# Kernel optimization log

Measured on AMD Instinct MI355X. Metric: run time of the kernel, lower is better.

The kernel has to match this reference:

```python
import jax, jax.numpy as jnp
import numpy as np

D = 1024
H = 16
F = 4096
EPS = 1e-6


def _layernorm(x, alpha, bias):
    # Faithful to torch: unbiased std (ddof=1), divide by (std + eps)
    mean = jnp.mean(x, axis=-1, keepdims=True)
    std = jnp.std(x, axis=-1, keepdims=True, ddof=1)
    return alpha * (x - mean) / (std + EPS) + bias


def setup_inputs() -> dict:
    key = jax.random.key(0)
    ks = jax.random.split(key, 12)
    B, S = 2, 2048
    s = 1.0 / np.sqrt(D)
    inp = {
        "x": jax.random.normal(ks[0], (B, S, D), jnp.float32),
        "mask": jnp.ones((B, 1, 1, S), jnp.int32),
        "wq": jax.random.normal(ks[1], (D, D), jnp.float32) * s,
        "bq": jnp.zeros((D,), jnp.float32),
        "wk": jax.random.normal(ks[2], (D, D), jnp.float32) * s,
        "bk": jnp.zeros((D,), jnp.float32),
        "wv": jax.random.normal(ks[3], (D, D), jnp.float32) * s,
        "bv": jnp.zeros((D,), jnp.float32),
        "wo": jax.random.normal(ks[4], (D, D), jnp.float32) * s,
        "bo": jnp.zeros((D,), jnp.float32),
        "ln1_a": jnp.ones((D,), jnp.float32),
        "ln1_b": jnp.zeros((D,), jnp.float32),
        "ln2_a": jnp.ones((D,), jnp.float32),
        "ln2_b": jnp.zeros((D,), jnp.float32),
        "w1": jax.random.normal(ks[5], (D, F), jnp.float32) * s,
        "b1": jnp.zeros((F,), jnp.float32),
        "w2": jax.random.normal(ks[6], (F, D), jnp.float32) * (1.0 / np.sqrt(F)),
        "b2": jnp.zeros((D,), jnp.float32),
    }
    return inp


def reference(x, mask, wq, bq, wk, bk, wv, bv, wo, bo,
              ln1_a, ln1_b, ln2_a, ln2_b, w1, b1, w2, b2):
    B, S, _ = x.shape
    dk = D // H
    # --- residual 1: pre-LN self-attention ---
    h = _layernorm(x, ln1_a, ln1_b)
    q = (h @ wq + bq).reshape(B, S, H, dk).transpose(0, 2, 1, 3)
    k = (h @ wk + bk).reshape(B, S, H, dk).transpose(0, 2, 1, 3)
    v = (h @ wv + bv).reshape(B, S, H, dk).transpose(0, 2, 1, 3)
    scores = jnp.einsum('bhqd,bhkd->bhqk', q, k) / jnp.sqrt(jnp.float32(dk))
    scores = jnp.where(mask == 0, jnp.float32(-1e9), scores)
    attn = jax.nn.softmax(scores, axis=-1)
    ctx = jnp.einsum('bhqk,bhkd->bhqd', attn, v)
    ctx = ctx.transpose(0, 2, 1, 3).reshape(B, S, D)
    x = x + (ctx @ wo + bo)
    # --- residual 2: pre-LN feed-forward ---
    h = _layernorm(x, ln2_a, ln2_b)
    ff = jax.nn.relu(h @ w1 + b1) @ w2 + b2
    return x + ff
```

## Files before the change

### kernel.cpp

```cpp
#include <hip/hip_runtime.h>
#include <hip/hip_bf16.h>

typedef __attribute__((ext_vector_type(8))) short bf16x8;
typedef __attribute__((ext_vector_type(4))) float f32x4;
typedef unsigned int uint32;

#define DMODEL 1024
#define SEQ    2048
#define NB     2
#define NH     16
#define HD     64
#define FDIM   4096
#define NTOK   (NB*SEQ)

__device__ __forceinline__ void async16(const void* g, void* s) {
    __builtin_amdgcn_global_load_lds((const __attribute__((address_space(1))) unsigned int*)g,
                                     (__attribute__((address_space(3))) unsigned int*)s,
                                     16, 0, 0);
}

__global__ __launch_bounds__(256) void transpose_cvt_k(const float* __restrict__ src,
                                                       __hip_bfloat16* __restrict__ dst,
                                                       int R, int C) {
    __shared__ __hip_bfloat16 tile[32][33];
    int tx = threadIdx.x, ty = threadIdx.y;
    int bx = blockIdx.x * 32, by = blockIdx.y * 32;
    for (int i = 0; i < 32; i += 8)
        tile[ty + i][tx] = __float2bfloat16(src[(size_t)(by + ty + i) * C + bx + tx]);
    __syncthreads();
    for (int i = 0; i < 32; i += 8)
        dst[(size_t)(bx + ty + i) * R + by + tx] = tile[tx][ty + i];
}

__global__ __launch_bounds__(256) void ln_kernel(const float* __restrict__ x,
                                                 const float* __restrict__ alpha,
                                                 const float* __restrict__ beta,
                                                 __hip_bfloat16* __restrict__ out) {
    const int row = blockIdx.x, tid = threadIdx.x;
    const size_t base = (size_t)row * DMODEL;
    float v[4];
    for (int e = 0; e < 4; ++e) v[e] = x[base + tid * 4 + e];
    float s1 = v[0] + v[1] + v[2] + v[3];
    float s2 = v[0]*v[0] + v[1]*v[1] + v[2]*v[2] + v[3]*v[3];
    for (int off = 32; off > 0; off >>= 1) {
        s1 += __shfl_down(s1, off);
        s2 += __shfl_down(s2, off);
    }
    __shared__ float red[8];
    int w = tid >> 6, lane = tid & 63;
    if (lane == 0) { red[w * 2] = s1; red[w * 2 + 1] = s2; }
    __syncthreads();
    if (tid == 0) {
        float a = 0.f, b = 0.f;
        for (int i = 0; i < 4; ++i) { a += red[2 * i]; b += red[2 * i + 1]; }
        red[0] = a; red[1] = b;
    }
    __syncthreads();
    s1 = red[0]; s2 = red[1];
    float mean = s1 * (1.0f / DMODEL);
    float var  = fmaxf((s2 - (float)DMODEL * mean * mean) * (1.0f / (DMODEL - 1)), 0.f);
    float inv  = 1.0f / (sqrtf(var) + 1e-6f);
    for (int e = 0; e < 4; ++e) {
        int c = tid * 4 + e;
        float y = alpha[c] * (v[e] - mean) * inv + beta[c];
        out[base + c] = __float2bfloat16(y);
    }
}

template <int EPI>
__global__ __launch_bounds__(256) void gemm_bt(const __hip_bfloat16* __restrict__ A,
                                               const __hip_bfloat16* __restrict__ Bt,
                                               const float* __restrict__ bias,
                                               const float* __restrict__ res,
                                               void* __restrict__ Cout,
                                               int M, int N, int K) {
    __shared__ alignas(16) __hip_bfloat16 As[2][128 * 32];
    __shared__ alignas(16) __hip_bfloat16 Bs[2][128 * 32];
    const int tid = threadIdx.x, l = tid & 63;
    const int w = tid >> 6;
    const int wm = w >> 1, wn = w & 1, quad = l >> 4, lc = l & 15;
    const int row0 = blockIdx.y * 128, col0 = blockIdx.x * 128;
    const int srow = 32 * w + (l >> 2), scol = (l & 3) * 8;

    f32x4 acc[4][4];
    for (int i = 0; i < 4; ++i)
        for (int j = 0; j < 4; ++j) acc[i][j] = (f32x4){0.f, 0.f, 0.f, 0.f};

    for (int c = 0; c < 2; ++c) {
        async16(A  + (size_t)(row0 + srow + 16 * c) * K + scol, (char*)&As[0][0] + w * 2048 + c * 1024);
        async16(Bt + (size_t)(col0 + srow + 16 * c) * K + scol, (char*)&Bs[0][0] + w * 2048 + c * 1024);
    }
    const int NKT = K / 32;
    for (int kt = 0; kt < NKT; ++kt) {
        const int cur = kt & 1;
        __syncthreads();
        if (kt + 1 < NKT) {
            const int k1 = (kt + 1) * 32;
            for (int c = 0; c < 2; ++c) {
                async16(A  + (size_t)(row0 + srow + 16 * c) * K + k1 + scol, (char*)&As[cur ^ 1][0] + w * 2048 + c * 1024);
                async16(Bt + (size_t)(col0 + srow + 16 * c) * K + k1 + scol, (char*)&Bs[cur ^ 1][0] + w * 2048 + c * 1024);
            }
        }
        bf16x8 af[4], bfr[4];
        for (int i = 0; i < 4; ++i) af[i]  = *(const bf16x8*)&As[cur][(64 * wm + 16 * i + lc) * 32 + quad * 8];
        for (int j = 0; j < 4; ++j) bfr[j] = *(const bf16x8*)&Bs[cur][(64 * wn + 16 * j + lc) * 32 + quad * 8];
        for (int i = 0; i < 4; ++i)
            for (int j = 0; j < 4; ++j)
                acc[i][j] = __builtin_amdgcn_mfma_f32_16x16x32_bf16(af[i], bfr[j], acc[i][j], 0, 0, 0);
    }

    __hip_bfloat16* Cb = (__hip_bfloat16*)Cout;
    float* Cf = (float*)Cout;
    for (int j = 0; j < 4; ++j) {
        int col = col0 + 64 * wn + 16 * j + lc;
        float bv = bias[col];
        for (int i = 0; i < 4; ++i) {
            int rbase = row0 + 64 * wm + 16 * i + quad * 4;
            for (int r = 0; r < 4; ++r) {
                size_t idx = (size_t)(rbase + r) * N + col;
                float vacc = acc[i][j][r] + bv;
                if (EPI == 0)      Cb[idx] = __float2bfloat16(vacc);
                else if (EPI == 1) Cb[idx] = __float2bfloat16(fmaxf(vacc, 0.f));
                else               Cf[idx] = vacc + res[idx];
            }
        }
    }
}

__global__ __launch_bounds__(256) void gemm_qkv(const __hip_bfloat16* __restrict__ A,
                                                const __hip_bfloat16* __restrict__ Bt,
                                                const float* __restrict__ bq,
                                                const float* __restrict__ bk,
                                                const float* __restrict__ bv,
                                                __hip_bfloat16* __restrict__ qout,
                                                __hip_bfloat16* __restrict__ kout,
                                                __hip_bfloat16* __restrict__ vTout) {
    const int K = DMODEL;
    __shared__ alignas(16) __hip_bfloat16 As[2][128 * 32];
    __shared__ alignas(16) __hip_bfloat16 Bs[2][128 * 32];
    const int tid = threadIdx.x, l = tid & 63;
    const int w = tid >> 6;
    const int wm = w >> 1, wn = w & 1, quad = l >> 4, lc = l & 15;
    const int row0 = blockIdx.y * 128, col0 = blockIdx.x * 128;
    const int srow = 32 * w + (l >> 2), scol = (l & 3) * 8;

    f32x4 acc[4][4];
    for (int i = 0; i < 4; ++i)
        for (int j = 0; j < 4; ++j) acc[i][j] = (f32x4){0.f, 0.f, 0.f, 0.f};

    for (int c = 0; c < 2; ++c) {
        async16(A  + (size_t)(row0 + srow + 16 * c) * K + scol, (char*)&As[0][0] + w * 2048 + c * 1024);
        async16(Bt + (size_t)(col0 + srow + 16 * c) * K + scol, (char*)&Bs[0][0] + w * 2048 + c * 1024);
    }
    const int NKT = K / 32;
    for (int kt = 0; kt < NKT; ++kt) {
        const int cur = kt & 1;
        __syncthreads();
        if (kt + 1 < NKT) {
            const int k1 = (kt + 1) * 32;
            for (int c = 0; c < 2; ++c) {
                async16(A  + (size_t)(row0 + srow + 16 * c) * K + k1 + scol, (char*)&As[cur ^ 1][0] + w * 2048 + c * 1024);
                async16(Bt + (size_t)(col0 + srow + 16 * c) * K + k1 + scol, (char*)&Bs[cur ^ 1][0] + w * 2048 + c * 1024);
            }
        }
        bf16x8 af[4], bfr[4];
        for (int i = 0; i < 4; ++i) af[i]  = *(const bf16x8*)&As[cur][(64 * wm + 16 * i + lc) * 32 + quad * 8];
        for (int j = 0; j < 4; ++j) bfr[j] = *(const bf16x8*)&Bs[cur][(64 * wn + 16 * j + lc) * 32 + quad * 8];
        for (int i = 0; i < 4; ++i)
            for (int j = 0; j < 4; ++j)
                acc[i][j] = __builtin_amdgcn_mfma_f32_16x16x32_bf16(af[i], bfr[j], acc[i][j], 0, 0, 0);
    }

    const int seg = col0 >> 10;
    const float* bias = (seg == 0) ? bq : (seg == 1) ? bk : bv;
    for (int j = 0; j < 4; ++j) {
        int col  = col0 + 64 * wn + 16 * j + lc;
        int colm = col & (DMODEL - 1);
        float bvx = bias[colm];
        for (int i = 0; i < 4; ++i) {
            int rbase = row0 + 64 * wm + 16 * i + quad * 4;
            for (int r = 0; r < 4; ++r) {
                int trow = rbase + r;
                float vacc = acc[i][j][r] + bvx;
                if (seg == 2) {
                    int bb = trow >> 11, s = trow & (SEQ - 1);
                    int hh = colm >> 6, d = colm & (HD - 1);
                    vTout[((size_t)(bb * NH + hh) * HD + d) * SEQ + s] = __float2bfloat16(vacc);
                } else {
                    __hip_bfloat16* dst = (seg == 0) ? qout : kout;
                    dst[(size_t)trow * DMODEL + colm] = __float2bfloat16(vacc);
                }
            }
        }
    }
}

__global__ __launch_bounds__(256) void attn_kernel(const __hip_bfloat16* __restrict__ q,
                                                   const __hip_bfloat16* __restrict__ k,
                                                   const __hip_bfloat16* __restrict__ vT,
                                                   const int* __restrict__ mask,
                                                   __hip_bfloat16* __restrict__ ctx) {
    const int qt = blockIdx.x, bh = blockIdx.y;
    const int b = bh >> 4;
    const int q0 = qt * 128;
    const int tid = threadIdx.x, w = tid >> 6, l = tid & 63, quad = l >> 4, lc = l & 15;

    __shared__ alignas(16) __hip_bfloat16 Kh[2][2][64 * 32];
    __shared__ alignas(16) __hip_bfloat16 Vh[2][2][64 * 32];

    const size_t base   = (size_t)b * SEQ * DMODEL + (size_t)(bh & 15) * HD;
    const size_t vtbase = (size_t)bh * HD * SEQ;

    bf16x8 qf[2][2];
    for (int s = 0; s < 2; ++s) {
        const __hip_bfloat16* qrow = &q[base + (size_t)(q0 + s * 64 + w * 16 + lc) * DMODEL];
        qf[s][0] = *(const bf16x8*)&qrow[quad * 8];
        qf[s][1] = *(const bf16x8*)&qrow[32 + quad * 8];
    }

    f32x4 o[2][4];
    for (int s = 0; s < 2; ++s)
        for (int dj = 0; dj < 4; ++dj) o[s][dj] = (f32x4){0.f, 0.f, 0.f, 0.f};
    float rsp2[2] = {0.f, 0.f};

    const int lr  = l >> 2, cb = l & 3;
    const int cbsw = ((cb ^ ((lr >> 1) & 3))) * 8;
    const int rsw  = (lc >> 1) & 3;
    const int b1v = (l >> 5) & 1, b0v = (l >> 4) & 1;

    for (int c = 0; c < 2; ++c) {
        const int W = w * 2 + c;
        const int rr = (W & 3) * 16 + lr, cc8 = (W >> 2) * 32 + cbsw;
        async16(&k [base   + (size_t)rr * DMODEL + cc8], (char*)&Kh[0][0][0] + W * 1024);
        async16(&vT[vtbase + (size_t)rr * SEQ + cc8],    (char*)&Vh[0][0][0] + W * 1024);
    }

    const int NT = SEQ / 64;
    for (int kt = 0; kt < NT; ++kt) {
        const int k0 = kt * 64;
        const int cur = kt & 1;

        __syncthreads();
        if (kt + 1 < NT) {
            const int k1 = k0 + 64;
            for (int c = 0; c < 2; ++c) {
                const int W = w * 2 + c;
                const int rr = (W & 3) * 16 + lr, cc8 = (W >> 2) * 32 + cbsw;
                async16(&k [base   + (size_t)(k1 + rr) * DMODEL + cc8], (char*)&Kh[cur ^ 1][0][0] + W * 1024);
                async16(&vT[vtbase + (size_t)rr * SEQ + k1 + cc8],      (char*)&Vh[cur ^ 1][0][0] + W * 1024);
            }
        }
        int4 mc[4];
        for (int jn = 0; jn < 4; ++jn)
            mc[jn] = *(const int4*)&mask[b * SEQ + k0 + jn * 16 + quad * 4];

        bf16x8 kf0[4], kf1[4];
        for (int jn = 0; jn < 4; ++jn) {
            kf0[jn] = *(const bf16x8*)&Kh[cur][0][(jn * 16 + lc) * 32 + (quad ^ rsw) * 8];
            kf1[jn] = *(const bf16x8*)&Kh[cur][1][(jn * 16 + lc) * 32 + (quad ^ rsw) * 8];
        }
        bf16x8 vf0[4], vf1[4];
        for (int dj = 0; dj < 4; ++dj) {
            vf0[dj] = *(const bf16x8*)&Vh[cur][0][(dj * 16 + lc) * 32 + (quad ^ rsw) * 8];
            vf1[dj] = *(const bf16x8*)&Vh[cur][1][(dj * 16 + lc) * 32 + (quad ^ rsw) * 8];
        }

        for (int s = 0; s < 2; ++s) {
            f32x4 sa[4];
            __builtin_amdgcn_s_setprio(1);
            for (int jn = 0; jn < 4; ++jn) {
                f32x4 z = (f32x4){0.f, 0.f, 0.f, 0.f};
                z = __builtin_amdgcn_mfma_f32_16x16x32_bf16(kf0[jn], qf[s][0], z, 0, 0, 0);
                z = __builtin_amdgcn_mfma_f32_16x16x32_bf16(kf1[jn], qf[s][1], z, 0, 0, 0);
                sa[jn] = z;
            }
            __builtin_amdgcn_s_setprio(0);

            uint32 wd[4][2];
            float accs = 0.f;
            for (int jn = 0; jn < 4; ++jn) {
                float p0 = mc[jn].x ? __expf(sa[jn][0] * 0.125f) : 0.f;
                float p1 = mc[jn].y ? __expf(sa[jn][1] * 0.125f) : 0.f;
                float p2 = mc[jn].z ? __expf(sa[jn][2] * 0.125f) : 0.f;
                float p3 = mc[jn].w ? __expf(sa[jn][3] * 0.125f) : 0.f;
                accs += (p0 + p1) + (p2 + p3);
                __hip_bfloat16 h0 = __float2bfloat16(p0), h1 = __float2bfloat16(p1);
                __hip_bfloat16 h2 = __float2bfloat16(p2), h3 = __float2bfloat16(p3);
                wd[jn][0] = (uint32)*(unsigned short*)&h0 | ((uint32)*(unsigned short*)&h1 << 16);
                wd[jn][1] = (uint32)*(unsigned short*)&h2 | ((uint32)*(unsigned short*)&h3 << 16);
            }
            rsp2[s] += accs;

            uint32 send1[4], kept[4];
            send1[0] = b1v ? wd[0][0] : wd[1][0];  kept[0] = b1v ? wd[1][0] : wd[0][0];
            send1[1] = b1v ? wd[0][1] : wd[1][1];  kept[1] = b1v ? wd[1][1] : wd[0][1];
            send1[2] = b1v ? wd[2][0] : wd[3][0];  kept[2] = b1v ? wd[3][0] : wd[2][0];
            send1[3] = b1v ? wd[2][1] : wd[3][1];  kept[3] = b1v ? wd[3][1] : wd[2][1];
            uint32 recv1[4];
            for (int t = 0; t < 4; ++t) recv1[t] = (uint32)__shfl_xor((int)send1[t], 32);
            uint32 send2[4], stay[4];
            for (int t = 0; t < 4; ++t) {
                send2[t] = (b1v == b0v) ? recv1[t] : kept[t];
                stay[t]  = (b1v == b0v) ? kept[t]  : recv1[t];
            }
            uint32 recv2[4];
            for (int t = 0; t < 4; ++t) recv2[t] = (uint32)__shfl_xor((int)send2[t], 16);
            uint32 G0[4], G1[4];
            for (int t = 0; t < 4; ++t) {
                G0[t] = b0v ? recv2[t] : stay[t];
                G1[t] = b0v ? stay[t]  : recv2[t];
            }
            union { uint32 u[4]; bf16x8 v8; } pf0, pf1;
            pf0.u[0] = G0[0]; pf0.u[1] = G0[1]; pf0.u[2] = G1[0]; pf0.u[3] = G1[1];
            pf1.u[0] = G0[2]; pf1.u[1] = G0[3]; pf1.u[2] = G1[2]; pf1.u[3] = G1[3];

            __builtin_amdgcn_s_setprio(1);
            for (int dj = 0; dj < 4; ++dj) {
                o[s][dj] = __builtin_amdgcn_mfma_f32_16x16x32_bf16(pf0.v8, vf0[dj], o[s][dj], 0, 0, 0);
                o[s][dj] = __builtin_amdgcn_mfma_f32_16x16x32_bf16(pf1.v8, vf1[dj], o[s][dj], 0, 0, 0);
            }
            __builtin_amdgcn_s_setprio(0);
        }
    }

    for (int s = 0; s < 2; ++s) {
        float rs = rsp2[s];
        rs += __shfl_xor(rs, 16);
        rs += __shfl_xor(rs, 32);
        for (int r = 0; r < 4; ++r) {
            float rq = __shfl(rs, (l & 48) | (quad * 4 + r));
            float linv = 1.0f / rq;
            int row = q0 + s * 64 + w * 16 + quad * 4 + r;
            for (int dj = 0; dj < 4; ++dj)
                ctx[base + (size_t)row * DMODEL + dj * 16 + lc] = __float2bfloat16(o[s][dj][r] * linv);
        }
    }
}

extern "C" void kernel_launch(void* const* d_in, const int* in_sizes, int n_in,
                              void* d_out, int out_size, void* d_ws, size_t ws_size,
                              hipStream_t stream) {
    const float* x    = (const float*)d_in[0];
    const int*   mask = (const int*)d_in[1];
    const float* wq = (const float*)d_in[2];
    const float* bq = (const float*)d_in[3];
    const float* wk = (const float*)d_in[4];
    const float* bk = (const float*)d_in[5];
    const float* wv = (const float*)d_in[6];
    const float* bv = (const float*)d_in[7];
    const float* wo = (const float*)d_in[8];
    const float* bo = (const float*)d_in[9];
    const float* ln1_a = (const float*)d_in[10];
    const float* ln1_b = (const float*)d_in[11];
    const float* ln2_a = (const float*)d_in[12];
    const float* ln2_b = (const float*)d_in[13];
    const float* w1 = (const float*)d_in[14];
    const float* b1 = (const float*)d_in[15];
    const float* w2 = (const float*)d_in[16];
    const float* b2 = (const float*)d_in[17];
    float* out = (float*)d_out;

    char* ws = (char*)d_ws;
    const size_t SZ_WT  = (size_t)DMODEL * DMODEL * 2;
    const size_t SZ_ACT = (size_t)NTOK * DMODEL * 2;
    const size_t SZ_WF  = (size_t)FDIM * DMODEL * 2;
    size_t off = 0;
    __hip_bfloat16* wqkvT = (__hip_bfloat16*)(ws + off); off += 3 * SZ_WT;
    __hip_bfloat16* woT   = (__hip_bfloat16*)(ws + off); off += SZ_WT;
    __hip_bfloat16* w1T   = (__hip_bfloat16*)(ws + off); off += SZ_WF;
    __hip_bfloat16* w2T   = (__hip_bfloat16*)(ws + off); off += SZ_WF;
    __hip_bfloat16* h1    = (__hip_bfloat16*)(ws + off); off += SZ_ACT;
    __hip_bfloat16* qb    = (__hip_bfloat16*)(ws + off); off += SZ_ACT;
    __hip_bfloat16* kb    = (__hip_bfloat16*)(ws + off); off += SZ_ACT;
    __hip_bfloat16* vTb   = (__hip_bfloat16*)(ws + off); off += SZ_ACT;
    __hip_bfloat16* ctx   = (__hip_bfloat16*)(ws + off); off += SZ_ACT;
    float*          x1    = (float*)(ws + off);          off += (size_t)NTOK * DMODEL * 4;
    __hip_bfloat16* h2    = (__hip_bfloat16*)(ws + off); off += SZ_ACT;
    __hip_bfloat16* ff1   = h1;

    dim3 tb(32, 8);
    transpose_cvt_k<<<dim3(32, 32), tb, 0, stream>>>(wq, wqkvT,                   DMODEL, DMODEL);
    transpose_cvt_k<<<dim3(32, 32), tb, 0, stream>>>(wk, wqkvT + 1024 * DMODEL,   DMODEL, DMODEL);
    transpose_cvt_k<<<dim3(32, 32), tb, 0, stream>>>(wv, wqkvT + 2048 * DMODEL,   DMODEL, DMODEL);
    transpose_cvt_k<<<dim3(32, 32), tb, 0, stream>>>(wo, woT, DMODEL, DMODEL);
    transpose_cvt_k<<<dim3(128, 32), tb, 0, stream>>>(w1, w1T, DMODEL, FDIM);
    transpose_cvt_k<<<dim3(32, 128), tb, 0, stream>>>(w2, w2T, FDIM, DMODEL);

    ln_kernel<<<NTOK, 256, 0, stream>>>(x, ln1_a, ln1_b, h1);

    gemm_qkv<<<dim3(3 * DMODEL / 128, NTOK / 128), 256, 0, stream>>>(h1, wqkvT, bq, bk, bv, qb, kb, vTb);

    attn_kernel<<<dim3(SEQ / 128, NB * NH), 256, 0, stream>>>(qb, kb, vTb, mask, ctx);

    gemm_bt<2><<<dim3(DMODEL / 128, NTOK / 128), 256, 0, stream>>>(ctx, woT, bo, x, x1, NTOK, DMODEL, DMODEL);

    ln_kernel<<<NTOK, 256, 0, stream>>>(x1, ln2_a, ln2_b, h2);

    gemm_bt<1><<<dim3(FDIM / 128, NTOK / 128), 256, 0, stream>>>(h2, w1T, b1, nullptr, ff1, NTOK, FDIM, DMODEL);
    gemm_bt<2><<<dim3(DMODEL / 128, NTOK / 128), 256, 0, stream>>>(ff1, w2T, b2, x1, out, NTOK, DMODEL, FDIM);
}
```

Before: 428.1 us.

## Swizzle GEMM LDS layout and split-K the N=1024 GEMMs within a block

Applies an XOR swizzle to the LDS tile layout in the GEMM kernels so the MFMA fragment reads avoid bank conflicts. Adds a 512-thread intra-block split-K GEMM in which two 4-wave groups each process half of K and combine their partial sums through shared memory. It is used for the output projection and the FFN down projection, whose grids have only 256 blocks, to raise the number of active waves. The cost is 64KB of LDS per block, which lowers block residency, plus an extra reduction phase.

```diff
diff --git a/kernel.cpp b/kernel.cpp
--- a/kernel.cpp
+++ b/kernel.cpp
@@ -80,7 +80,10 @@
     const int w = tid >> 6;
     const int wm = w >> 1, wn = w & 1, quad = l >> 4, lc = l & 15;
     const int row0 = blockIdx.y * 128, col0 = blockIdx.x * 128;
-    const int srow = 32 * w + (l >> 2), scol = (l & 3) * 8;
+    const int lr = l >> 2, cb = l & 3;
+    const int srow = 32 * w + lr;
+    const int scol = (cb ^ ((lr >> 1) & 3)) * 8;
+    const int rsw  = (lc >> 1) & 3;
 
     f32x4 acc[4][4];
     for (int i = 0; i < 4; ++i)
@@ -102,8 +105,8 @@
             }
         }
         bf16x8 af[4], bfr[4];
-        for (int i = 0; i < 4; ++i) af[i]  = *(const bf16x8*)&As[cur][(64 * wm + 16 * i + lc) * 32 + quad * 8];
-        for (int j = 0; j < 4; ++j) bfr[j] = *(const bf16x8*)&Bs[cur][(64 * wn + 16 * j + lc) * 32 + quad * 8];
+        for (int i = 0; i < 4; ++i) af[i]  = *(const bf16x8*)&As[cur][(64 * wm + 16 * i + lc) * 32 + (quad ^ rsw) * 8];
+        for (int j = 0; j < 4; ++j) bfr[j] = *(const bf16x8*)&Bs[cur][(64 * wn + 16 * j + lc) * 32 + (quad ^ rsw) * 8];
         for (int i = 0; i < 4; ++i)
             for (int j = 0; j < 4; ++j)
                 acc[i][j] = __builtin_amdgcn_mfma_f32_16x16x32_bf16(af[i], bfr[j], acc[i][j], 0, 0, 0);
@@ -122,6 +125,95 @@
                 if (EPI == 0)      Cb[idx] = __float2bfloat16(vacc);
                 else if (EPI == 1) Cb[idx] = __float2bfloat16(fmaxf(vacc, 0.f));
                 else               Cf[idx] = vacc + res[idx];
+            }
+        }
+    }
+}
+
+template <int EPI>
+__global__ __launch_bounds__(512) void gemm_bt_sk(const __hip_bfloat16* __restrict__ A,
+                                                  const __hip_bfloat16* __restrict__ Bt,
+                                                  const float* __restrict__ bias,
+                                                  const float* __restrict__ res,
+                                                  void* __restrict__ Cout,
+                                                  int M, int N, int K) {
+    __shared__ alignas(16) char smem[65536];
+    const int tid = threadIdx.x, l = tid & 63;
+    const int w = tid >> 6;
+    const int g = w >> 2;
+    const int wl = w & 3;
+    const int wm = wl >> 1, wn = wl & 1, quad = l >> 4, lc = l & 15;
+    const int row0 = blockIdx.y * 128, col0 = blockIdx.x * 128;
+    const int lr = l >> 2, cb = l & 3;
+    const int srow = 32 * wl + lr;
+    const int scol = (cb ^ ((lr >> 1) & 3)) * 8;
+    const int rsw  = (lc >> 1) & 3;
+    const int Kh = K >> 1;
+    const int kbase = g * Kh;
+
+    char* AsBase = smem + (size_t)g * 16384;
+    char* BsBase = smem + 32768 + (size_t)g * 16384;
+
+    f32x4 acc[4][4];
+    for (int i = 0; i < 4; ++i)
+        for (int j = 0; j < 4; ++j) acc[i][j] = (f32x4){0.f, 0.f, 0.f, 0.f};
+
+    for (int c = 0; c < 2; ++c) {
+        async16(A  + (size_t)(row0 + srow + 16 * c) * K + kbase + scol, AsBase + wl * 2048 + c * 1024);
+        async16(Bt + (size_t)(col0 + srow + 16 * c) * K + kbase + scol, BsBase + wl * 2048 + c * 1024);
+    }
+    const int NKT = Kh / 32;
+    for (int kt = 0; kt < NKT; ++kt) {
+        const int cur = kt & 1;
+        __syncthreads();
+        if (kt + 1 < NKT) {
+            const int k1 = kbase + (kt + 1) * 32;
+            for (int c = 0; c < 2; ++c) {
+                async16(A  + (size_t)(row0 + srow + 16 * c) * K + k1 + scol, AsBase + (cur ^ 1) * 8192 + wl * 2048 + c * 1024);
+                async16(Bt + (size_t)(col0 + srow + 16 * c) * K + k1 + scol, BsBase + (cur ^ 1) * 8192 + wl * 2048 + c * 1024);
+            }
+        }
+        const __hip_bfloat16* Asc = (const __hip_bfloat16*)(AsBase + cur * 8192);
+        const __hip_bfloat16* Bsc = (const __hip_bfloat16*)(BsBase + cur * 8192);
+        bf16x8 af[4], bfr[4];
+        for (int i = 0; i < 4; ++i) af[i]  = *(const bf16x8*)&Asc[(64 * wm + 16 * i + lc) * 32 + (quad ^ rsw) * 8];
+        for (int j = 0; j < 4; ++j) bfr[j] = *(const bf16x8*)&Bsc[(64 * wn + 16 * j + lc) * 32 + (quad ^ rsw) * 8];
+        for (int i = 0; i < 4; ++i)
+            for (int j = 0; j < 4; ++j)
+                acc[i][j] = __builtin_amdgcn_mfma_f32_16x16x32_bf16(af[i], bfr[j], acc[i][j], 0, 0, 0);
+    }
+
+    __syncthreads();
+    float* comb = (float*)smem;
+    if (g == 1) {
+        for (int j = 0; j < 4; ++j) {
+            int col = 64 * wn + 16 * j + lc;
+            int ccol = col ^ ((quad & 1) << 4);
+            for (int i = 0; i < 4; ++i) {
+                int rb = 64 * wm + 16 * i + quad * 4;
+                for (int r = 0; r < 4; ++r)
+                    comb[(rb + r) * 128 + ccol] = acc[i][j][r];
+            }
+        }
+    }
+    __syncthreads();
+    if (g == 0) {
+        __hip_bfloat16* Cb = (__hip_bfloat16*)Cout;
+        float* Cf = (float*)Cout;
+        for (int j = 0; j < 4; ++j) {
+            int coll = 64 * wn + 16 * j + lc;
+            int ccol = coll ^ ((quad & 1) << 4);
+            int col  = col0 + coll;
+            float bv = bias[col];
+            for (int i = 0; i < 4; ++i) {
+                int rbl = 64 * wm + 16 * i + quad * 4;
+                for (int r = 0; r < 4; ++r) {
+                    size_t idx = (size_t)(row0 + rbl + r) * N + col;
+                    float vacc = acc[i][j][r] + comb[(rbl + r) * 128 + ccol] + bv;
+                    if (EPI == 0)      Cb[idx] = __float2bfloat16(vacc);
+                    else if (EPI == 1) Cb[idx] = __float2bfloat16(fmaxf(vacc, 0.f));
+                    else               Cf[idx] = vacc + res[idx];
+                }
             }
         }
     }
@@ -142,7 +234,10 @@
     const int w = tid >> 6;
     const int wm = w >> 1, wn = w & 1, quad = l >> 4, lc = l & 15;
     const int row0 = blockIdx.y * 128, col0 = blockIdx.x * 128;
-    const int srow = 32 * w + (l >> 2), scol = (l & 3) * 8;
+    const int lr = l >> 2, cb = l & 3;
+    const int srow = 32 * w + lr;
+    const int scol = (cb ^ ((lr >> 1) & 3)) * 8;
+    const int rsw  = (lc >> 1) & 3;
 
     f32x4 acc[4][4];
     for (int i = 0; i < 4; ++i)
@@ -164,8 +259,8 @@
             }
         }
         bf16x8 af[4], bfr[4];
-        for (int i = 0; i < 4; ++i) af[i]  = *(const bf16x8*)&As[cur][(64 * wm + 16 * i + lc) * 32 + quad * 8];
-        for (int j = 0; j < 4; ++j) bfr[j] = *(const bf16x8*)&Bs[cur][(64 * wn + 16 * j + lc) * 32 + quad * 8];
+        for (int i = 0; i < 4; ++i) af[i]  = *(const bf16x8*)&As[cur][(64 * wm + 16 * i + lc) * 32 + (quad ^ rsw) * 8];
+        for (int j = 0; j < 4; ++j) bfr[j] = *(const bf16x8*)&Bs[cur][(64 * wn + 16 * j + lc) * 32 + (quad ^ rsw) * 8];
         for (int i = 0; i < 4; ++i)
             for (int j = 0; j < 4; ++j)
                 acc[i][j] = __builtin_amdgcn_mfma_f32_16x16x32_bf16(af[i], bfr[j], acc[i][j], 0, 0, 0);
@@ -392,10 +487,10 @@
 
     attn_kernel<<<dim3(SEQ / 128, NB * NH), 256, 0, stream>>>(qb, kb, vTb, mask, ctx);
 
-    gemm_bt<2><<<dim3(DMODEL / 128, NTOK / 128), 256, 0, stream>>>(ctx, woT, bo, x, x1, NTOK, DMODEL, DMODEL);
+    gemm_bt_sk<2><<<dim3(DMODEL / 128, NTOK / 128), 512, 0, stream>>>(ctx, woT, bo, x, x1, NTOK, DMODEL, DMODEL);
 
     ln_kernel<<<NTOK, 256, 0, stream>>>(x1, ln2_a, ln2_b, h2);
 
     gemm_bt<1><<<dim3(FDIM / 128, NTOK / 128), 256, 0, stream>>>(h2, w1T, b1, nullptr, ff1, NTOK, FDIM, DMODEL);
-    gemm_bt<2><<<dim3(DMODEL / 128, NTOK / 128), 256, 0, stream>>>(ff1, w2T, b2, x1, out, NTOK, DMODEL, FDIM);
-}
+    gemm_bt_sk<2><<<dim3(DMODEL / 128, NTOK / 128), 512, 0, stream>>>(ff1, w2T, b2, x1, out, NTOK, DMODEL, FDIM);
+}
```

Measured after the change: 400.4 us. -6.5%, faster.
